# Performance work log

Measured on AMD Instinct MI355X. Metric: run time of the kernel, lower is better.

The kernel has to match this reference:

```python
import jax, jax.numpy as jnp
import numpy as np
from itertools import product

NUM_LEVELS = 4
NUM_FEATURES = 4
B, L = 32, 512

def build_kernel(num_features, num_levels):
    # signatory.all_words ordering: words grouped by length 1..num_levels, lexicographic within length
    words = [w for m in range(1, num_levels + 1) for w in product(range(num_features), repeat=m)]
    num_components = num_levels * (num_levels + 1) // 2
    k = np.zeros((num_components, num_features, len(words)), dtype=np.float32)
    for i, word in enumerate(words):
        m = len(word)
        start = m * (m - 1) // 2
        for j, axis in enumerate(word):
            k[start + j, axis, i] = 1.0
    return jnp.asarray(k)

def setup_inputs() -> dict:
    key = jax.random.key(0)
    x = jax.random.normal(key, (B, L, NUM_FEATURES), dtype=jnp.float32)
    return {"x": x, "kernel": build_kernel(NUM_FEATURES, NUM_LEVELS)}

def reference(x, kernel):
    Bn, Ln, F = x.shape
    NF = kernel.shape[-1]  # num_functionals = 340
    # path increments
    seq = x[:, 1:, :] - x[:, :-1, :]                      # (B, L-1, F)
    # lift: (C, B, L-1, NF), C = num_levels*(num_levels+1)/2 = 10
    M = jnp.einsum('blf,cfk->cblk', seq, kernel)
    # level-by-level recursion with independent weights, return_sequences=True
    # then summed over the stacked level axis (stack+sum == running sum of Y terms)
    sig = jnp.cumsum(M[0], axis=1)                        # level 1
    k = 1
    for m in range(1, NUM_LEVELS):
        R = M[k]; k += 1
        for _ in range(m):
            # tf.cumsum(..., exclusive=True) == inclusive cumsum minus self
            R = M[k] * (jnp.cumsum(R, axis=1) - R)
            k += 1
        sig = sig + jnp.cumsum(R, axis=1)
    # prepend zero time step -> (B, L, NF)
    sig = jnp.concatenate([jnp.zeros((Bn, 1, NF), dtype=x.dtype), sig], axis=1)
    # prepend constant-1 functional channel -> (B, L, NF+1)
    return jnp.concatenate([jnp.ones((Bn, Ln, 1), dtype=x.dtype), sig], axis=-1)
```

## Files before the change

kernel.cpp:

```cpp
#include <hip/hip_runtime.h>


#define SIG_B 32
#define SIG_L 512
#define SIG_NSTEP 511
#define SIG_ROW 341
#define SIG_CS 32
#define SIG_C 16
#define SIG_PAD 344

__global__ __launch_bounds__(256) void sigA(const float* __restrict__ x,
                                            float* __restrict__ Lsig) {
    const int bc = blockIdx.x;
    const int b = bc / SIG_C, c = bc % SIG_C;
    const int tid = threadIdx.x;
    const int t0 = c * SIG_CS;
    const int nt = min(SIG_CS, SIG_NSTEP - t0);

    __shared__ float dlds[SIG_CS * 4];
    const float* xb = x + ((size_t)b * SIG_L + t0) * 4;
    if (tid < SIG_CS) {
        float4 d = make_float4(0.f, 0.f, 0.f, 0.f);
        if (tid < nt) {
            float4 x0 = *(const float4*)(xb + tid * 4);
            float4 x1 = *(const float4*)(xb + (tid + 1) * 4);
            d = make_float4(x1.x - x0.x, x1.y - x0.y, x1.z - x0.z, x1.w - x0.w);
        }
        *(float4*)(dlds + tid * 4) = d;
    }
    __syncthreads();

    const int a = tid >> 6, bb = (tid >> 4) & 3, cc = (tid >> 2) & 3, ee = tid & 3;
    float s1 = 0.f, s2 = 0.f, s3 = 0.f, s4 = 0.f;
#pragma unroll
    for (int t = 0; t < SIG_CS; ++t) {
        const float* dp = dlds + t * 4;
        const float da = dp[a], db = dp[bb], dc = dp[cc], de = dp[ee];
        s4 = fmaf(s3, de, s4);
        s3 = fmaf(s2, dc, s3);
        s2 = fmaf(s1, db, s2);
        s1 += da;
    }
    float* Lr = Lsig + (size_t)bc * SIG_PAD;
    if ((tid & 63) == 0) Lr[1 + a] = s1;
    if ((tid & 15) == 0) Lr[5 + (tid >> 4)] = s2;
    if ((tid & 3) == 0)  Lr[21 + (tid >> 2)] = s3;
    Lr[85 + tid] = s4;
}

__global__ __launch_bounds__(256) void sigC(const float* __restrict__ x,
                                            const float* __restrict__ Lsig,
                                            float* __restrict__ out) {
    const int bc = blockIdx.x;
    const int b = bc / SIG_C, c = bc % SIG_C;
    const int tid = threadIdx.x;
    const int t0 = c * SIG_CS;
    const int nt = min(SIG_CS, SIG_NSTEP - t0);

    __shared__ float dlds[SIG_CS * 4];
    __shared__ float L[SIG_C * SIG_PAD];

    const float* xb = x + ((size_t)b * SIG_L + t0) * 4;
    if (tid < SIG_CS) {
        float4 d = make_float4(0.f, 0.f, 0.f, 0.f);
        if (tid < nt) {
            float4 x0 = *(const float4*)(xb + tid * 4);
            float4 x1 = *(const float4*)(xb + (tid + 1) * 4);
            d = make_float4(x1.x - x0.x, x1.y - x0.y, x1.z - x0.z, x1.w - x0.w);
        }
        *(float4*)(dlds + tid * 4) = d;
    }
    {
        const float4* Lb4 = (const float4*)(Lsig + (size_t)b * SIG_C * SIG_PAD);
        float4* L4p = (float4*)L;
        const int n4 = c * (SIG_PAD / 4);
        for (int i = tid; i < n4; i += 256) L4p[i] = Lb4[i];
    }
    __syncthreads();

    const int a = tid >> 6, bb = (tid >> 4) & 3, cc = (tid >> 2) & 3, ee = tid & 3;

    float p1 = 0.f, p2 = 0.f, p3 = 0.f, p4 = 0.f;
    for (int j = 0; j < c; ++j) {
        const float* Lc = L + j * SIG_PAD;
        const float l1a = Lc[1 + a], l1b = Lc[1 + bb], l1c = Lc[1 + cc], l1e = Lc[1 + ee];
        const float l2ab = Lc[5 + 4 * a + bb], l2bc = Lc[5 + 4 * bb + cc],
                    l2ce = Lc[5 + 4 * cc + ee];
        const float l3abc = Lc[21 + 16 * a + 4 * bb + cc],
                    l3bce = Lc[21 + 16 * bb + 4 * cc + ee];
        const float l4 = Lc[85 + tid];
        p4 += p3 * l1e + p2 * l2ce + p1 * l3bce + l4;
        p3 += p2 * l1c + p1 * l2bc + l3abc;
        p2 += p1 * l1b + l2ab;
        p1 += l1a;
    }

    float* row = out + ((size_t)b * SIG_L + (t0 + 1)) * SIG_ROW;

    if (c == 0) {
        float* r0 = out + (size_t)b * SIG_L * SIG_ROW;
        if (tid == 0)        __builtin_nontemporal_store(1.0f, r0 + 0);
        if ((tid & 63) == 0) __builtin_nontemporal_store(0.f, r0 + 1 + a);
        if ((tid & 15) == 0) __builtin_nontemporal_store(0.f, r0 + 5 + (tid >> 4));
        if ((tid & 3) == 0)  __builtin_nontemporal_store(0.f, r0 + 21 + (tid >> 2));
        __builtin_nontemporal_store(0.f, r0 + 85 + tid);
    }

#pragma unroll
    for (int t = 0; t < SIG_CS; ++t) {
        const float* dp = dlds + t * 4;
        const float da = dp[a], db = dp[bb], dc = dp[cc], de = dp[ee];
        p4 = fmaf(p3, de, p4);
        p3 = fmaf(p2, dc, p3);
        p2 = fmaf(p1, db, p2);
        p1 += da;

        if (t < nt) {
            float* r = row + (size_t)t * SIG_ROW;
            if (tid == 0)        __builtin_nontemporal_store(1.0f, r + 0);
            if ((tid & 63) == 0) __builtin_nontemporal_store(p1, r + 1 + a);
            if ((tid & 15) == 0) __builtin_nontemporal_store(p2, r + 5 + (tid >> 4));
            if ((tid & 3) == 0)  __builtin_nontemporal_store(p3, r + 21 + (tid >> 2));
            __builtin_nontemporal_store(p4, r + 85 + tid);
        }
    }
}

extern "C" void kernel_launch(void* const* d_in, const int* in_sizes, int n_in,
                              void* d_out, int out_size, void* d_ws, size_t ws_size,
                              hipStream_t stream) {
    const float* x = (const float*)d_in[0];
    float* out = (float*)d_out;
    float* Lsig = (float*)d_ws;

    sigA<<<SIG_B * SIG_C, 256, 0, stream>>>(x, Lsig);
    sigC<<<SIG_B * SIG_C, 256, 0, stream>>>(x, Lsig, out);
}
```

Baseline: 22.03 us.

## Process four interleaved chunks per block to raise ILP and share prefix combine

```diff
diff --git a/kernel.cpp b/kernel.cpp
--- a/kernel.cpp
+++ b/kernel.cpp
@@ -7,81 +7,103 @@
 #define SIG_ROW 341
 #define SIG_CS 32
 #define SIG_C 16
+#define SIG_G 4
 #define SIG_PAD 344
 
-__global__ __launch_bounds__(256) void sigA(const float* __restrict__ x,
-                                            float* __restrict__ Lsig) {
-    const int bc = blockIdx.x;
-    const int b = bc / SIG_C, c = bc % SIG_C;
-    const int tid = threadIdx.x;
-    const int t0 = c * SIG_CS;
-    const int nt = min(SIG_CS, SIG_NSTEP - t0);
-
-    __shared__ float dlds[SIG_CS * 4];
-    const float* xb = x + ((size_t)b * SIG_L + t0) * 4;
-    if (tid < SIG_CS) {
+__device__ __forceinline__ void stage4(const float* __restrict__ xb,
+                                       float* dlds, int tid, int g) {
+    if (tid < 128) {
+        const int k = tid >> 5, t = tid & 31;
+        const int gt = (g + 4 * k) * SIG_CS + t;
         float4 d = make_float4(0.f, 0.f, 0.f, 0.f);
-        if (tid < nt) {
-            float4 x0 = *(const float4*)(xb + tid * 4);
-            float4 x1 = *(const float4*)(xb + (tid + 1) * 4);
+        if (gt < SIG_NSTEP) {
+            float4 x0 = *(const float4*)(xb + gt * 4);
+            float4 x1 = *(const float4*)(xb + gt * 4 + 4);
             d = make_float4(x1.x - x0.x, x1.y - x0.y, x1.z - x0.z, x1.w - x0.w);
         }
-        *(float4*)(dlds + tid * 4) = d;
+        *(float4*)(dlds + (k * SIG_CS + t) * 4) = d;
     }
+}
+
+#define SIG_CHAIN_STEP(K, S1, S2, S3, S4)                                   \
+    do {                                                                    \
+        const float* dp_ = dlds + ((K) * SIG_CS + t) * 4;                   \
+        const float da_ = dp_[a], db_ = dp_[bb], dc_ = dp_[cc], de_ = dp_[ee];\
+        S4 = fmaf(S3, de_, S4);      \
+        S3 = fmaf(S2, dc_, S3);                                             \
+        S2 = fmaf(S1, db_, S2);                                             \
+        S1 += da_;                                                          \
+    } while (0)
+
+__global__ __launch_bounds__(256) void sigA4(const float* __restrict__ x,
+                                             float* __restrict__ Lsig) {
+    const int b = blockIdx.x >> 2, g = blockIdx.x & 3;
+    const int tid = threadIdx.x;
+
+    __shared__ float dlds[SIG_G * SIG_CS * 4];
+    stage4(x + (size_t)b * SIG_L * 4, dlds, tid, g);
     __syncthreads();
 
     const int a = tid >> 6, bb = (tid >> 4) & 3, cc = (tid >> 2) & 3, ee = tid & 3;
-    float s1 = 0.f, s2 = 0.f, s3 = 0.f, s4 = 0.f;
-#pragma unroll
+
+    float s1_0 = 0.f, s2_0 = 0.f, s3_0 = 0.f, s4_0 = 0.f;
+    float s1_1 = 0.f, s2_1 = 0.f, s3_1 = 0.f, s4_1 = 0.f;
+    float s1_2 = 0.f, s2_2 = 0.f, s3_2 = 0.f, s4_2 = 0.f;
+    float s1_3 = 0.f, s2_3 = 0.f, s3_3 = 0.f, s4_3 = 0.f;
+
+#pragma unroll 4
     for (int t = 0; t < SIG_CS; ++t) {
-        const float* dp = dlds + t * 4;
-        const float da = dp[a], db = dp[bb], dc = dp[cc], de = dp[ee];
-        s4 = fmaf(s3, de, s4);
-        s3 = fmaf(s2, dc, s3);
-        s2 = fmaf(s1, db, s2);
-        s1 += da;
+        SIG_CHAIN_STEP(0, s1_0, s2_0, s3_0, s4_0);
+        SIG_CHAIN_STEP(1, s1_1, s2_1, s3_1, s4_1);
+        SIG_CHAIN_STEP(2, s1_2, s2_2, s3_2, s4_2);
+        SIG_CHAIN_STEP(3, s1_3, s2_3, s3_3, s4_3);
     }
-    float* Lr = Lsig + (size_t)bc * SIG_PAD;
-    if ((tid & 63) == 0) Lr[1 + a] = s1;
-    if ((tid & 15) == 0) Lr[5 + (tid >> 4)] = s2;
-    if ((tid & 3) == 0)  Lr[21 + (tid >> 2)] = s3;
-    Lr[85 + tid] = s4;
+
+#define SIG_WRITE_L(K, S1, S2, S3, S4)                                      \
+    do {                                                                    \
+        float* Lr = Lsig + (size_t)(b * SIG_C + g + 4 * (K)) * SIG_PAD;     \
+        if ((tid & 63) == 0) Lr[1 + a] = S1;                                \
+        if ((tid & 15) == 0) Lr[5 + (tid >> 4)] = S2;                       \
+        if ((tid & 3) == 0)  Lr[21 + (tid >> 2)] = S3;                      \
+        Lr[85 + tid] = S4;                                                  \
+    } while (0)
+
+    SIG_WRITE_L(0, s1_0, s2_0, s3_0, s4_0);
+    SIG_WRITE_L(1, s1_1, s2_1, s3_1, s4_1);
+    SIG_WRITE_L(2, s1_2, s2_2, s3_2, s4_2);
+    SIG_WRITE_L(3, s1_3, s2_3, s3_3, s4_3);
+#undef SIG_WRITE_L
 }
 
-__global__ __launch_bounds__(256) void sigC(const float* __restrict__ x,
-                                            const float* __restrict__ Lsig,
-                                            float* __restrict__ out) {
-    const int bc = blockIdx.x;
-    const int b = bc / SIG_C, c = bc % SIG_C;
+__global__ __launch_bounds__(256) void sigC4(const float* __restrict__ x,
+                                             const float* __restrict__ Lsig,
+                                             float* __restrict__ out) {
+    const int b = blockIdx.x >> 2, g = blockIdx.x & 3;
     const int tid = threadIdx.x;
-    const int t0 = c * SIG_CS;
-    const int nt = min(SIG_CS, SIG_NSTEP - t0);
 
-    __shared__ float dlds[SIG_CS * 4];
-    __shared__ float L[SIG_C * SIG_PAD];
+    __shared__ float dlds[SIG_G * SIG_CS * 4];
+    __shared__ float L[(SIG_C - 1) * SIG_PAD];
 
-    const float* xb = x + ((size_t)b * SIG_L + t0) * 4;
-    if (tid < SIG_CS) {
-        float4 d = make_float4(0.f, 0.f, 0.f, 0.f);
-        if (tid < nt) {
-            float4 x0 = *(const float4*)(xb + tid * 4);
-            float4 x1 = *(const float4*)(xb + (tid + 1) * 4);
-            d = make_float4(x1.x - x0.x, x1.y - x0.y, x1.z - x0.z, x1.w - x0.w);
-        }
-        *(float4*)(dlds + tid * 4) = d;
-    }
+    stage4(x + (size_t)b * SIG_L * 4, dlds, tid, g);
     {
         const float4* Lb4 = (const float4*)(Lsig + (size_t)b * SIG_C * SIG_PAD);
         float4* L4p = (float4*)L;
-        const int n4 = c * (SIG_PAD / 4);
+        const int n4 = (SIG_C - 1) * (SIG_PAD / 4);
         for (int i = tid; i < n4; i += 256) L4p[i] = Lb4[i];
     }
     __syncthreads();
 
     const int a = tid >> 6, bb = (tid >> 4) & 3, cc = (tid >> 2) & 3, ee = tid & 3;
+    const int c0 = g, c1 = g + 4, c2 = g + 8, c3 = g + 12;
 
     float p1 = 0.f, p2 = 0.f, p3 = 0.f, p4 = 0.f;
-    for (int j = 0; j < c; ++j) {
+    float q1_0, q2_0, q3_0, q4_0, q1_1, q2_1, q3_1, q4_1;
+    float q1_2, q2_2, q3_2, q4_2, q1_3, q2_3, q3_3, q4_3;
+    for (int j = 0; j < SIG_C - 1; ++j) {
+        if (j == c0) { q1_0 = p1; q2_0 = p2; q3_0 = p3; q4_0 = p4; }
+        if (j == c1) { q1_1 = p1; q2_1 = p2; q3_1 = p3; q4_1 = p4; }
+        if (j == c2) { q1_2 = p1; q2_2 = p2; q3_2 = p3; q4_2 = p4; }
+        if (j == c3) { q1_3 = p1; q2_3 = p2; q3_3 = p3; q4_3 = p4; }
         const float* Lc = L + j * SIG_PAD;
         const float l1a = Lc[1 + a], l1b = Lc[1 + bb], l1c = Lc[1 + cc], l1e = Lc[1 + ee];
         const float l2ab = Lc[5 + 4 * a + bb], l2bc = Lc[5 + 4 * bb + cc],
@@ -94,10 +116,9 @@
         p2 += p1 * l1b + l2ab;
         p1 += l1a;
     }
+    if (c3 == SIG_C - 1) { q1_3 = p1; q2_3 = p2; q3_3 = p3; q4_3 = p4; }
 
-    float* row = out + ((size_t)b * SIG_L + (t0 + 1)) * SIG_ROW;
-
-    if (c == 0) {
+    if (g == 0) {
         float* r0 = out + (size_t)b * SIG_L * SIG_ROW;
         if (tid == 0)        __builtin_nontemporal_store(1.0f, r0 + 0);
         if ((tid & 63) == 0) __builtin_nontemporal_store(0.f, r0 + 1 + a);
@@ -106,24 +127,35 @@
         __builtin_nontemporal_store(0.f, r0 + 85 + tid);
     }
 
-#pragma unroll
+    float* row0p = out + ((size_t)b * SIG_L + c0 * SIG_CS + 1) * SIG_ROW;
+    float* row1p = out + ((size_t)b * SIG_L + c1 * SIG_CS + 1) * SIG_ROW;
+    float* row2p = out + ((size_t)b * SIG_L + c2 * SIG_CS + 1) * SIG_ROW;
+    float* row3p = out + ((size_t)b * SIG_L + c3 * SIG_CS + 1) * SIG_ROW;
+    const bool last3 = (c3 == SIG_C - 1);
+
+#define SIG_STORE_ROW(RP, S1, S2, S3, S4)                                    \
+    do {                                                                     \
+        float* r_ = (RP) + (size_t)t * SIG_ROW;                              \
+        if (tid == 0)        __builtin_nontemporal_store(1.0f, r_ + 0);      \
+        if ((tid & 63) == 0) __builtin_nontemporal_store(S1, r_ + 1 + a);    \
+        if ((tid & 15) == 0) __builtin_nontemporal_store(S2, r_ + 5 + (tid >> 4)); \
+        if ((tid & 3) == 0)  __builtin_nontemporal_store(S3, r_ + 21 + (tid >> 2)); \
+        __builtin_nontemporal_store(S4, r_ + 85 + tid);                      \
+    } while (0)
+
+#pragma unroll 4
     for (int t = 0; t < SIG_CS; ++t) {
-        const float* dp = dlds + t * 4;
-        const float da = dp[a], db = dp[bb], dc = dp[cc], de = dp[ee];
-        p4 = fmaf(p3, de, p4);
-        p3 = fmaf(p2, dc, p3);
-        p2 = fmaf(p1, db, p2);
-        p1 += da;
-
-        if (t < nt) {
-            float* r = row + (size_t)t * SIG_ROW;
-            if (tid == 0)        __builtin_nontemporal_store(1.0f, r + 0);
-            if ((tid & 63) == 0) __builtin_nontemporal_store(p1, r + 1 + a);
-            if ((tid & 15) == 0) __builtin_nontemporal_store(p2, r + 5 + (tid >> 4));
-            if ((tid & 3) == 0)  __builtin_nontemporal_store(p3, r + 21 + (tid >> 2));
-            __builtin_nontemporal_store(p4, r + 85 + tid);
-        }
+        SIG_CHAIN_STEP(0, q1_0, q2_0, q3_0, q4_0);
+        SIG_CHAIN_STEP(1, q1_1, q2_1, q3_1, q4_1);
+        SIG_CHAIN_STEP(2, q1_2, q2_2, q3_2, q4_2);
+        SIG_CHAIN_STEP(3, q1_3, q2_3, q3_3, q4_3);
+        SIG_STORE_ROW(row0p, q1_0, q2_0, q3_0, q4_0);
+        SIG_STORE_ROW(row1p, q1_1, q2_1, q3_1, q4_1);
+        SIG_STORE_ROW(row2p, q1_2, q2_2, q3_2, q4_2);
+        if (!last3 || t < SIG_CS - 1)
+            SIG_STORE_ROW(row3p, q1_3, q2_3, q3_3, q4_3);
     }
+#undef SIG_STORE_ROW
 }
 
 extern "C" void kernel_launch(void* const* d_in, const int* in_sizes, int n_in,
@@ -133,6 +165,6 @@
     float* out = (float*)d_out;
     float* Lsig = (float*)d_ws;
 
-    sigA<<<SIG_B * SIG_C, 256, 0, stream>>>(x, Lsig);
-    sigC<<<SIG_B * SIG_C, 256, 0, stream>>>(x, Lsig, out);
+    sigA4<<<SIG_B * SIG_G, 256, 0, stream>>>(x, Lsig);
+    sigC4<<<SIG_B * SIG_G, 256, 0, stream>>>(x, Lsig, out);
 }
```

New measurement: 32.79 us. 48.8% more time.
